# Optimization experiments

Measured on AMD Instinct MI355X. Metric: run time of the kernel, lower is better.

Reference implementation:

```python
import jax, jax.numpy as jnp
import numpy as np

ALPHA = 1.0   # init alpha=1 -> temporal (TDI) term has zero weight
GAMMA = 0.01  # soft-min temperature
INF = 1e9     # finite stand-in for +inf boundary of the DP matrix


def setup_inputs() -> dict:
    key = jax.random.key(0)
    k1, k2 = jax.random.split(key)
    B, N, F = 64, 512, 1
    return {
        "input": jax.random.normal(k1, (B, N, F), dtype=jnp.float32),
        "target": jax.random.normal(k2, (B, N, F), dtype=jnp.float32),
    }


def _soft_dtw(D, gamma):
    """Batched soft-DTW value via anti-diagonal wavefront scan.

    D: (B, n, n) cost matrix. Returns (B,) soft-DTW values R[n, n].
    Recursion: R[i,j] = D[i-1,j-1] + softmin_gamma(R[i-1,j-1], R[i-1,j], R[i,j-1]).
    """
    B, n, _ = D.shape
    ii = jnp.arange(n + 1)           # row index i of diagonal entries
    ic = jnp.clip(ii - 1, 0, n - 1)  # clipped cost-row index (masked below)
    inf_row = jnp.full((B, n + 1), INF, D.dtype)
    diag_d0 = inf_row.at[:, 0].set(0.0)  # R[0,0]=0, rest inf
    diag_d1 = inf_row                    # R[1,0]=R[0,1]=inf
    pad_col = jnp.full((B, 1), INF, D.dtype)

    def step(carry, d):
        r2, r1 = carry  # diagonals d-2, d-1, indexed by i in [0, n]
        jj = d - ii
        jc = jnp.clip(jj - 1, 0, n - 1)
        dvals = D[:, ic, jc]  # (B, n+1) costs along diagonal d
        r2s = jnp.concatenate([pad_col, r2[:, :-1]], axis=1)  # R[i-1, j-1]
        r1s = jnp.concatenate([pad_col, r1[:, :-1]], axis=1)  # R[i-1, j]
        # softmin_gamma(a,b,c) = -gamma * logsumexp(-[a,b,c]/gamma)
        cand = jnp.stack([-r2s, -r1s, -r1], axis=0) / gamma
        smin = -gamma * jax.nn.logsumexp(cand, axis=0)
        valid = (ii >= 1) & (ii <= n) & (jj >= 1) & (jj <= n)
        new = jnp.where(valid[None, :], dvals + smin, INF)
        return (r1, new), None

    (_, last), _ = jax.lax.scan(step, (diag_d0, diag_d1), jnp.arange(2, 2 * n + 1))
    return last[:, n]  # R[n, n] per batch element


def reference(input, target):
    # derivative DILATE: operate on first differences of the series
    dx = input[:, 1:, :] - input[:, :-1, :]   # (B, n, F), n = N-1
    dy = target[:, 1:, :] - target[:, :-1, :]
    # pairwise squared-Euclidean cost D[b, i, j] = ||dy_i - dx_j||^2
    D = jnp.sum((dy[:, :, None, :] - dx[:, None, :, :]) ** 2, axis=-1)
    loss_shape = jnp.mean(_soft_dtw(D, GAMMA))
    # DILATE = alpha * loss_shape + (1 - alpha) * loss_temporal; alpha == 1 here,
    # so the TDI (temporal) term has zero weight and is omitted.
    return ALPHA * loss_shape
```

## Files before the change

### kernel.cpp

```cpp
#include <hip/hip_runtime.h>
#include <math.h>


#define INF_F 1000000000.0f

typedef float v4f __attribute__((ext_vector_type(4)));

__device__ __forceinline__ float dpp_shr1_inj(float x, float oldv){
  int r = __builtin_amdgcn_update_dpp(__float_as_int(oldv), __float_as_int(x),
                                      0x138 , 0xf, 0xf, false);
  return __int_as_float(r);
}
__device__ __forceinline__ float min3f(float a, float b, float c){
  float d;
  asm("v_min3_f32 %0, %1, %2, %3" : "=v"(d) : "v"(a), "v"(b), "v"(c));
  return d;
}
#define PINF(v) asm volatile("" : "+v"(v))

#define LOADW(P, B2) { const float2* _p = dxe2 + (B2); \
  float2 a0=_p[0],a1=_p[1],a2=_p[2],a3=_p[3],a4=_p[4],a5=_p[5],a6=_p[6],a7=_p[7]; \
  float2 a8=_p[8],a9=_p[9],a10=_p[10],a11=_p[11],a12=_p[12],a13=_p[13]; \
  float2 a14=_p[14],a15=_p[15],a16=_p[16]; \
  P##0=a0.x;  P##1=a0.y;  P##2=a1.x;  P##3=a1.y;  P##4=a2.x;  P##5=a2.y; \
  P##6=a3.x;  P##7=a3.y;  P##8=a4.x;  P##9=a4.y;  P##10=a5.x; P##11=a5.y; \
  P##12=a6.x; P##13=a6.y; P##14=a7.x; P##15=a7.y; P##16=a8.x; P##17=a8.y; \
  P##18=a9.x; P##19=a9.y; P##20=a10.x;P##21=a10.y;P##22=a11.x;P##23=a11.y; \
  P##24=a12.x;P##25=a12.y;P##26=a13.x;P##27=a13.y;P##28=a14.x;P##29=a14.y; \
  P##30=a15.x;P##31=a15.y;P##32=a16.x;P##33=a16.y; }

#define PINW(P) { PINF(P##0); PINF(P##1); PINF(P##2); PINF(P##3); PINF(P##4); \
  PINF(P##5); PINF(P##6); PINF(P##7); PINF(P##8); PINF(P##9); PINF(P##10); \
  PINF(P##11); PINF(P##12); PINF(P##13); PINF(P##14); PINF(P##15); PINF(P##16); \
  PINF(P##17); PINF(P##18); PINF(P##19); PINF(P##20); PINF(P##21); PINF(P##22); \
  PINF(P##23); PINF(P##24); PINF(P##25); PINF(P##26); PINF(P##27); PINF(P##28); \
  PINF(P##29); PINF(P##30); PINF(P##31); PINF(P##32); PINF(P##33); }

#define STEP2(K, MB, XLO, XHI) { \
  float sh1 = dpp_shr1_inj(r1_hi, (MB)); \
  float uL  = dy_lo - (XLO); \
  float uH  = dy_hi - (XHI); \
  float nv_hi = fmaf(uH, uH, min3f(r2_lo, r1_lo, r1_hi)); \
  float nv_lo = fmaf(uL, uL, min3f(SH2, sh1, r1_lo)); \
  pb##K = nv_hi; \
  if ((K) == 28) { if (cc == 31) ans = nv_hi; } \
  SH2 = sh1; r2_lo = r1_lo; r1_lo = nv_lo; r1_hi = nv_hi; }

#define CHUNK(C, XU, XP) { \
  const int cc = (C); \
  if (w > 0) { \
    while (__hip_atomic_load(&flagz[w-1], __ATOMIC_ACQUIRE, \
                             __HIP_MEMORY_SCOPE_WORKGROUP) <= cc) { \
      __builtin_amdgcn_s_sleep(1); \
    } \
    const v4f* Mr = (const v4f*)&Mbx[w][32*cc]; \
    q0 = Mr[0]; q1 = Mr[1]; q2 = Mr[2]; q3 = Mr[3]; \
    q4 = Mr[4]; q5 = Mr[5]; q6 = Mr[6]; q7 = Mr[7]; \
    m32v = Mbx[w][32*cc+32]; \
    PINF(q0); PINF(q1); PINF(q2); PINF(q3); \
    PINF(q4); PINF(q5); PINF(q6); PINF(q7); PINF(m32v); \
  } \
  PINW(XU); \
  LOADW(XP, 257 + 16*(cc+1) - t); \
  asm volatile("" ::: "memory"); \
  STEP2(0,  q0.y,  XU##1,  XU##0 ) STEP2(1,  q0.z,  XU##2,  XU##1 ) \
  STEP2(2,  q0.w,  XU##3,  XU##2 ) STEP2(3,  q1.x,  XU##4,  XU##3 ) \
  STEP2(4,  q1.y,  XU##5,  XU##4 ) STEP2(5,  q1.z,  XU##6,  XU##5 ) \
  STEP2(6,  q1.w,  XU##7,  XU##6 ) STEP2(7,  q2.x,  XU##8,  XU##7 ) \
  STEP2(8,  q2.y,  XU##9,  XU##8 ) STEP2(9,  q2.z,  XU##10, XU##9 ) \
  STEP2(10, q2.w,  XU##11, XU##10) STEP2(11, q3.x,  XU##12, XU##11) \
  STEP2(12, q3.y,  XU##13, XU##12) STEP2(13, q3.z,  XU##14, XU##13) \
  STEP2(14, q3.w,  XU##15, XU##14) STEP2(15, q4.x,  XU##16, XU##15) \
  STEP2(16, q4.y,  XU##17, XU##16) STEP2(17, q4.z,  XU##18, XU##17) \
  STEP2(18, q4.w,  XU##19, XU##18) STEP2(19, q5.x,  XU##20, XU##19) \
  STEP2(20, q5.y,  XU##21, XU##20) STEP2(21, q5.z,  XU##22, XU##21) \
  STEP2(22, q5.w,  XU##23, XU##22) STEP2(23, q6.x,  XU##24, XU##23) \
  STEP2(24, q6.y,  XU##25, XU##24) STEP2(25, q6.z,  XU##26, XU##25) \
  STEP2(26, q6.w,  XU##27, XU##26) STEP2(27, q7.x,  XU##28, XU##27) \
  STEP2(28, q7.y,  XU##29, XU##28) STEP2(29, q7.z,  XU##30, XU##29) \
  STEP2(30, q7.w,  XU##31, XU##30) STEP2(31, m32v,  XU##32, XU##31) \
  if (w < 3) { \
    if (lane == 63) { \
      float2* Pd = (float2*)&Mbx[w+1][32*cc+2]; \
      Pd[0]  = make_float2(pb0,  pb1);  Pd[1]  = make_float2(pb2,  pb3); \
      Pd[2]  = make_float2(pb4,  pb5);  Pd[3]  = make_float2(pb6,  pb7); \
      Pd[4]  = make_float2(pb8,  pb9);  Pd[5]  = make_float2(pb10, pb11); \
      Pd[6]  = make_float2(pb12, pb13); Pd[7]  = make_float2(pb14, pb15); \
      Pd[8]  = make_float2(pb16, pb17); Pd[9]  = make_float2(pb18, pb19); \
      Pd[10] = make_float2(pb20, pb21); Pd[11] = make_float2(pb22, pb23); \
      Pd[12] = make_float2(pb24, pb25); Pd[13] = make_float2(pb26, pb27); \
      Pd[14] = make_float2(pb28, pb29); Pd[15] = make_float2(pb30, pb31); \
    } \
    __hip_atomic_store(&flagz[w], cc+1, __ATOMIC_RELEASE, \
                       __HIP_MEMORY_SCOPE_WORKGROUP); \
  } }

__global__ __launch_bounds__(256, 1)
void sdtw_kernel(const float* __restrict__ input,
                 const float* __restrict__ target,
                 float* __restrict__ out) {
  const int b = blockIdx.x;
  const int t = threadIdx.x;
  const int w = t >> 6;
  const int lane = t & 63;

  __shared__ __align__(8) float dxe[1576];
  __shared__ __align__(16) float Mbx[4][1040];
  __shared__ int flagz[4];

  const float* __restrict__ inp = input + b * 512;
  const float* __restrict__ tgt = target + b * 512;

  for (int idx = t; idx < 1576; idx += 256) {
    float v = 0.0f;
    if (idx >= 514 && idx <= 1024) v = inp[idx - 513] - inp[idx - 514];
    dxe[idx] = v;
  }
  for (int k2 = t; k2 < 4 * 1040; k2 += 256) (&Mbx[0][0])[k2] = INF_F;
  if (t < 4) flagz[t] = 0;

  float dy_lo = (t >= 1) ? (tgt[2*t] - tgt[2*t - 1]) : 0.0f;
  float dy_hi = tgt[2*t + 1] - tgt[2*t];

  float r1_lo = INF_F, r1_hi = INF_F;
  float r2_lo = (t == 0) ? 0.0f : INF_F;
  float SH2   = INF_F;

  v4f q0 = {INF_F, INF_F, INF_F, INF_F};
  v4f q1 = q0, q2 = q0, q3 = q0, q4 = q0, q5 = q0, q6 = q0, q7 = q0;
  float m32v = INF_F;
  float pb0,  pb1,  pb2,  pb3,  pb4,  pb5,  pb6,  pb7;
  float pb8,  pb9,  pb10, pb11, pb12, pb13, pb14, pb15;
  float pb16, pb17, pb18, pb19, pb20, pb21, pb22, pb23;
  float pb24, pb25, pb26, pb27, pb28, pb29, pb30, pb31;
  float xa0,xa1,xa2,xa3,xa4,xa5,xa6,xa7,xa8,xa9,xa10,xa11,xa12,xa13,xa14,xa15;
  float xa16,xa17,xa18,xa19,xa20,xa21,xa22,xa23,xa24,xa25,xa26,xa27,xa28,xa29;
  float xa30,xa31,xa32,xa33;
  float xb0,xb1,xb2,xb3,xb4,xb5,xb6,xb7,xb8,xb9,xb10,xb11,xb12,xb13,xb14,xb15;
  float xb16,xb17,xb18,xb19,xb20,xb21,xb22,xb23,xb24,xb25,xb26,xb27,xb28,xb29;
  float xb30,xb31,xb32,xb33;

  float ans = INF_F;
  const float2* dxe2 = (const float2*)dxe;

  __syncthreads();

  LOADW(xa, 257 - t);

#pragma unroll 1
  for (int c = 0; c < 32; c += 2) {
    CHUNK(c,     xa, xb)
    CHUNK(c + 1, xb, xa)
  }

  if (w == 3 && lane == 63) {
    atomicAdd(out, ans * (1.0f / 64.0f));
  }
}

extern "C" void kernel_launch(void* const* d_in, const int* in_sizes, int n_in,
                              void* d_out, int out_size, void* d_ws, size_t ws_size,
                              hipStream_t stream) {
  const float* input  = (const float*)d_in[0];
  const float* target = (const float*)d_in[1];
  float* out = (float*)d_out;

  hipMemsetAsync(out, 0, sizeof(float), stream);
  sdtw_kernel<<<64, 256, 0, stream>>>(input, target, out);
}
```

Measured before the change: 85.82 us.

## Process four DP rows per thread with two wavefronts instead of four

Each thread now owns four consecutive rows of the DP matrix instead of two, so a block needs 128 threads (two wavefronts) rather than 256. This halves the number of cross-wave handoffs through shared memory and the flag spin-waits along the wavefront pipeline. In exchange, each diagonal step carries a longer serial min3/fma chain per thread and needs more registers for the wider window of dx values.

```diff
diff --git a/kernel.cpp b/kernel.cpp
--- a/kernel.cpp
+++ b/kernel.cpp
@@ -21,67 +21,89 @@
 #define LOADW(P, B2) { const float2* _p = dxe2 + (B2); \
   float2 a0=_p[0],a1=_p[1],a2=_p[2],a3=_p[3],a4=_p[4],a5=_p[5],a6=_p[6],a7=_p[7]; \
   float2 a8=_p[8],a9=_p[9],a10=_p[10],a11=_p[11],a12=_p[12],a13=_p[13]; \
-  float2 a14=_p[14],a15=_p[15],a16=_p[16]; \
+  float2 a14=_p[14],a15=_p[15],a16=_p[16],a17=_p[17]; \
   P##0=a0.x;  P##1=a0.y;  P##2=a1.x;  P##3=a1.y;  P##4=a2.x;  P##5=a2.y; \
   P##6=a3.x;  P##7=a3.y;  P##8=a4.x;  P##9=a4.y;  P##10=a5.x; P##11=a5.y; \
   P##12=a6.x; P##13=a6.y; P##14=a7.x; P##15=a7.y; P##16=a8.x; P##17=a8.y; \
   P##18=a9.x; P##19=a9.y; P##20=a10.x;P##21=a10.y;P##22=a11.x;P##23=a11.y; \
   P##24=a12.x;P##25=a12.y;P##26=a13.x;P##27=a13.y;P##28=a14.x;P##29=a14.y; \
-  P##30=a15.x;P##31=a15.y;P##32=a16.x;P##33=a16.y; }
+  P##30=a15.x;P##31=a15.y;P##32=a16.x;P##33=a16.y;P##34=a17.x;P##35=a17.y; }
 
 #define PINW(P) { PINF(P##0); PINF(P##1); PINF(P##2); PINF(P##3); PINF(P##4); \
   PINF(P##5); PINF(P##6); PINF(P##7); PINF(P##8); PINF(P##9); PINF(P##10); \
   PINF(P##11); PINF(P##12); PINF(P##13); PINF(P##14); PINF(P##15); PINF(P##16); \
   PINF(P##17); PINF(P##18); PINF(P##19); PINF(P##20); PINF(P##21); PINF(P##22); \
   PINF(P##23); PINF(P##24); PINF(P##25); PINF(P##26); PINF(P##27); PINF(P##28); \
-  PINF(P##29); PINF(P##30); PINF(P##31); PINF(P##32); PINF(P##33); }
+  PINF(P##29); PINF(P##30); PINF(P##31); PINF(P##32); PINF(P##33); PINF(P##34); \
+  PINF(P##35); }
 
-#define STEP2(K, MB, XLO, XHI) { \
-  float sh1 = dpp_shr1_inj(r1_hi, (MB)); \
-  float uL  = dy_lo - (XLO); \
-  float uH  = dy_hi - (XHI); \
-  float nv_hi = fmaf(uH, uH, min3f(r2_lo, r1_lo, r1_hi)); \
-  float nv_lo = fmaf(uL, uL, min3f(SH2, sh1, r1_lo)); \
-  pb##K = nv_hi; \
-  if ((K) == 28) { if (cc == 31) ans = nv_hi; } \
-  SH2 = sh1; r2_lo = r1_lo; r1_lo = nv_lo; r1_hi = nv_hi; }
+#define STEP4(K, MB, X3, X2, X1, X0) { \
+  float sh1 = dpp_shr1_inj(A3, (MB)); \
+  float u0 = dy0 - (X3); \
+  float u1 = dy1 - (X2); \
+  float u2 = dy2 - (X1); \
+  float u3 = dy3 - (X0); \
+  float nv0 = fmaf(u0, u0, min3f(SH2, sh1, A0)); \
+  float nv1 = fmaf(u1, u1, min3f(B0, A0, A1)); \
+  float nv2 = fmaf(u2, u2, min3f(B1, A1, A2)); \
+  float nv3 = fmaf(u3, u3, min3f(B2, A2, A3)); \
+  pb##K = nv3; \
+  if ((K) == 28) { if (cc == 31) ans = nv3; } \
+  SH2 = sh1; B0 = A0; B1 = A1; B2 = A2; \
+  A0 = nv0; A1 = nv1; A2 = nv2; A3 = nv3; }
 
 #define CHUNK(C, XU, XP) { \
   const int cc = (C); \
   if (w > 0) { \
-    while (__hip_atomic_load(&flagz[w-1], __ATOMIC_ACQUIRE, \
+    while (__hip_atomic_load(&flagz[0], __ATOMIC_ACQUIRE, \
                              __HIP_MEMORY_SCOPE_WORKGROUP) <= cc) { \
       __builtin_amdgcn_s_sleep(1); \
     } \
-    const v4f* Mr = (const v4f*)&Mbx[w][32*cc]; \
+    const v4f* Mr = (const v4f*)&Mbx[32*cc]; \
     q0 = Mr[0]; q1 = Mr[1]; q2 = Mr[2]; q3 = Mr[3]; \
     q4 = Mr[4]; q5 = Mr[5]; q6 = Mr[6]; q7 = Mr[7]; \
-    m32v = Mbx[w][32*cc+32]; \
+    m32v = Mbx[32*cc+32]; \
     PINF(q0); PINF(q1); PINF(q2); PINF(q3); \
     PINF(q4); PINF(q5); PINF(q6); PINF(q7); PINF(m32v); \
   } \
   PINW(XU); \
-  LOADW(XP, 257 + 16*(cc+1) - t); \
+  LOADW(XP, 257 + 16*(cc+1) - 2*t); \
   asm volatile("" ::: "memory"); \
-  STEP2(0,  q0.y,  XU##1,  XU##0 ) STEP2(1,  q0.z,  XU##2,  XU##1 ) \
-  STEP2(2,  q0.w,  XU##3,  XU##2 ) STEP2(3,  q1.x,  XU##4,  XU##3 ) \
-  STEP2(4,  q1.y,  XU##5,  XU##4 ) STEP2(5,  q1.z,  XU##6,  XU##5 ) \
-  STEP2(6,  q1.w,  XU##7,  XU##6 ) STEP2(7,  q2.x,  XU##8,  XU##7 ) \
-  STEP2(8,  q2.y,  XU##9,  XU##8 ) STEP2(9,  q2.z,  XU##10, XU##9 ) \
-  STEP2(10, q2.w,  XU##11, XU##10) STEP2(11, q3.x,  XU##12, XU##11) \
-  STEP2(12, q3.y,  XU##13, XU##12) STEP2(13, q3.z,  XU##14, XU##13) \
-  STEP2(14, q3.w,  XU##15, XU##14) STEP2(15, q4.x,  XU##16, XU##15) \
-  STEP2(16, q4.y,  XU##17, XU##16) STEP2(17, q4.z,  XU##18, XU##17) \
-  STEP2(18, q4.w,  XU##19, XU##18) STEP2(19, q5.x,  XU##20, XU##19) \
-  STEP2(20, q5.y,  XU##21, XU##20) STEP2(21, q5.z,  XU##22, XU##21) \
-  STEP2(22, q5.w,  XU##23, XU##22) STEP2(23, q6.x,  XU##24, XU##23) \
-  STEP2(24, q6.y,  XU##25, XU##24) STEP2(25, q6.z,  XU##26, XU##25) \
-  STEP2(26, q6.w,  XU##27, XU##26) STEP2(27, q7.x,  XU##28, XU##27) \
-  STEP2(28, q7.y,  XU##29, XU##28) STEP2(29, q7.z,  XU##30, XU##29) \
-  STEP2(30, q7.w,  XU##31, XU##30) STEP2(31, m32v,  XU##32, XU##31) \
-  if (w < 3) { \
+  STEP4(0,  q0.y, XU##3,  XU##2,  XU##1,  XU##0 ) \
+  STEP4(1,  q0.z, XU##4,  XU##3,  XU##2,  XU##1 ) \
+  STEP4(2,  q0.w, XU##5,  XU##4,  XU##3,  XU##2 ) \
+  STEP4(3,  q1.x, XU##6,  XU##5,  XU##4,  XU##3 ) \
+  STEP4(4,  q1.y, XU##7,  XU##6,  XU##5,  XU##4 ) \
+  STEP4(5,  q1.z, XU##8,  XU##7,  XU##6,  XU##5 ) \
+  STEP4(6,  q1.w, XU##9,  XU##8,  XU##7,  XU##6 ) \
+  STEP4(7,  q2.x, XU##10, XU##9,  XU##8,  XU##7 ) \
+  STEP4(8,  q2.y, XU##11, XU##10, XU##9,  XU##8 ) \
+  STEP4(9,  q2.z, XU##12, XU##11, XU##10, XU##9 ) \
+  STEP4(10, q2.w, XU##13, XU##12, XU##11, XU##10) \
+  STEP4(11, q3.x, XU##14, XU##13, XU##12, XU##11) \
+  STEP4(12, q3.y, XU##15, XU##14, XU##13, XU##12) \
+  STEP4(13, q3.z, XU##16, XU##15, XU##14, XU##13) \
+  STEP4(14, q3.w, XU##17, XU##16, XU##15, XU##14) \
+  STEP4(15, q4.x, XU##18, XU##17, XU##16, XU##15) \
+  STEP4(16, q4.y, XU##19, XU##18, XU##17, XU##16) \
+  STEP4(17, q4.z, XU##20, XU##19, XU##18, XU##17) \
+  STEP4(18, q4.w, XU##21, XU##20, XU##19, XU##18) \
+  STEP4(19, q5.x, XU##22, XU##21, XU##20, XU##19) \
+  STEP4(20, q5.y, XU##23, XU##22, XU##21, XU##20) \
+  STEP4(21, q5.z, XU##24, XU##23, XU##22, XU##21) \
+  STEP4(22, q5.w, XU##25, XU##24, XU##23, XU##22) \
+  STEP4(23, q6.x, XU##26, XU##25, XU##24, XU##23) \
+  STEP4(24, q6.y, XU##27, XU##26, XU##25, XU##24) \
+  STEP4(25, q6.z, XU##28, XU##27, XU##26, XU##25) \
+  STEP4(26, q6.w, XU##29, XU##28, XU##27, XU##26) \
+  STEP4(27, q7.x, XU##30, XU##29, XU##28, XU##27) \
+  STEP4(28, q7.y, XU##31, XU##30, XU##29, XU##28) \
+  STEP4(29, q7.z, XU##32, XU##31, XU##30, XU##29) \
+  STEP4(30, q7.w, XU##33, XU##32, XU##31, XU##30) \
+  STEP4(31, m32v, XU##34, XU##33, XU##32, XU##31) \
+  if (w < 1) { \
     if (lane == 63) { \
-      float2* Pd = (float2*)&Mbx[w+1][32*cc+2]; \
+      float2* Pd = (float2*)&Mbx[32*cc+2]; \
       Pd[0]  = make_float2(pb0,  pb1);  Pd[1]  = make_float2(pb2,  pb3); \
       Pd[2]  = make_float2(pb4,  pb5);  Pd[3]  = make_float2(pb6,  pb7); \
       Pd[4]  = make_float2(pb8,  pb9);  Pd[5]  = make_float2(pb10, pb11); \
@@ -91,11 +113,11 @@
       Pd[12] = make_float2(pb24, pb25); Pd[13] = make_float2(pb26, pb27); \
       Pd[14] = make_float2(pb28, pb29); Pd[15] = make_float2(pb30, pb31); \
     } \
-    __hip_atomic_store(&flagz[w], cc+1, __ATOMIC_RELEASE, \
+    __hip_atomic_store(&flagz[0], cc+1, __ATOMIC_RELEASE, \
                        __HIP_MEMORY_SCOPE_WORKGROUP); \
   } }
 
-__global__ __launch_bounds__(256, 1)
+__global__ __launch_bounds__(128, 1)
 void sdtw_kernel(const float* __restrict__ input,
                  const float* __restrict__ target,
                  float* __restrict__ out) {
@@ -105,26 +127,29 @@
   const int lane = t & 63;
 
   __shared__ __align__(8) float dxe[1576];
-  __shared__ __align__(16) float Mbx[4][1040];
-  __shared__ int flagz[4];
+  __shared__ __align__(16) float Mbx[1040];
+  __shared__ int flagz[1];
 
   const float* __restrict__ inp = input + b * 512;
   const float* __restrict__ tgt = target + b * 512;
 
-  for (int idx = t; idx < 1576; idx += 256) {
+  for (int idx = t; idx < 1576; idx += 128) {
     float v = 0.0f;
-    if (idx >= 514 && idx <= 1024) v = inp[idx - 513] - inp[idx - 514];
+    if (idx >= 516 && idx <= 1026) v = inp[idx - 515] - inp[idx - 516];
     dxe[idx] = v;
   }
-  for (int k2 = t; k2 < 4 * 1040; k2 += 256) (&Mbx[0][0])[k2] = INF_F;
-  if (t < 4) flagz[t] = 0;
+  for (int k2 = t; k2 < 1040; k2 += 128) Mbx[k2] = INF_F;
+  if (t == 0) flagz[0] = 0;
 
-  float dy_lo = (t >= 1) ? (tgt[2*t] - tgt[2*t - 1]) : 0.0f;
-  float dy_hi = tgt[2*t + 1] - tgt[2*t];
+  float dy0 = (t >= 1) ? (tgt[4*t]     - tgt[4*t - 1]) : 0.0f;
+  float dy1 =            tgt[4*t + 1] - tgt[4*t];
+  float dy2 =            tgt[4*t + 2] - tgt[4*t + 1];
+  float dy3 =            tgt[4*t + 3] - tgt[4*t + 2];
 
-  float r1_lo = INF_F, r1_hi = INF_F;
-  float r2_lo = (t == 0) ? 0.0f : INF_F;
-  float SH2   = INF_F;
+  float A0 = INF_F, A1 = INF_F, A2 = INF_F, A3 = INF_F;
+  float B0 = (t == 0) ? 0.0f : INF_F;
+  float B1 = INF_F, B2 = INF_F;
+  float SH2 = INF_F;
 
   v4f q0 = {INF_F, INF_F, INF_F, INF_F};
   v4f q1 = q0, q2 = q0, q3 = q0, q4 = q0, q5 = q0, q6 = q0, q7 = q0;
@@ -135,17 +160,17 @@
   float pb24, pb25, pb26, pb27, pb28, pb29, pb30, pb31;
   float xa0,xa1,xa2,xa3,xa4,xa5,xa6,xa7,xa8,xa9,xa10,xa11,xa12,xa13,xa14,xa15;
   float xa16,xa17,xa18,xa19,xa20,xa21,xa22,xa23,xa24,xa25,xa26,xa27,xa28,xa29;
-  float xa30,xa31,xa32,xa33;
+  float xa30,xa31,xa32,xa33,xa34,xa35;
   float xb0,xb1,xb2,xb3,xb4,xb5,xb6,xb7,xb8,xb9,xb10,xb11,xb12,xb13,xb14,xb15;
   float xb16,xb17,xb18,xb19,xb20,xb21,xb22,xb23,xb24,xb25,xb26,xb27,xb28,xb29;
-  float xb30,xb31,xb32,xb33;
+  float xb30,xb31,xb32,xb33,xb34,xb35;
 
   float ans = INF_F;
   const float2* dxe2 = (const float2*)dxe;
 
   __syncthreads();
 
-  LOADW(xa, 257 - t);
+  LOADW(xa, 257 - 2*t);
 
 #pragma unroll 1
   for (int c = 0; c < 32; c += 2) {
@@ -153,7 +178,7 @@
     CHUNK(c + 1, xb, xa)
   }
 
-  if (w == 3 && lane == 63) {
+  if (w == 1 && lane == 63) {
     atomicAdd(out, ans * (1.0f / 64.0f));
   }
 }
@@ -166,5 +191,5 @@
   float* out = (float*)d_out;
 
   hipMemsetAsync(out, 0, sizeof(float), stream);
-  sdtw_kernel<<<64, 256, 0, stream>>>(input, target, out);
+  sdtw_kernel<<<64, 128, 0, stream>>>(input, target, out);
 }
```

New measurement: 91.21 us. 1.06x slower.
